# Performance work log

Measured on AMD Instinct MI355X. Metric: run time of the kernel, lower is better.

## Reference

```python
import jax, jax.numpy as jnp
import numpy as np

N, E, IN, OUT = 50000, 800000, 256, 256
EPS = 1e-5


def setup_inputs() -> dict:
    key = jax.random.key(0)
    k1, k2, k3 = jax.random.split(key, 3)
    x = jax.random.normal(k1, (N, IN), dtype=jnp.float32)
    edge_index = jax.random.randint(k2, (2, E), 0, N, dtype=jnp.int64)
    batch = jnp.zeros((N,), dtype=jnp.int64)
    # glorot-style init for GCN weight
    scale = jnp.sqrt(2.0 / (IN + OUT)).astype(jnp.float32)
    W = jax.random.normal(k3, (IN, OUT), dtype=jnp.float32) * scale
    conv_bias = jnp.zeros((OUT,), dtype=jnp.float32)
    ln_weight = jnp.ones((OUT,), dtype=jnp.float32)
    ln_bias = jnp.zeros((OUT,), dtype=jnp.float32)
    prelu_a = jnp.full((1,), 0.25, dtype=jnp.float32)  # nn.PReLU default
    return {"x": x, "edge_index": edge_index, "batch": batch, "W": W,
            "conv_bias": conv_bias, "ln_weight": ln_weight,
            "ln_bias": ln_bias, "prelu_a": prelu_a}


def reference(x, edge_index, batch, W, conv_bias, ln_weight, ln_bias, prelu_a):
    n = x.shape[0]
    src, dst = edge_index[0], edge_index[1]
    # GCNConv: add self-loops, symmetric deg^{-1/2} normalization
    loop = jnp.arange(n, dtype=src.dtype)
    src_f = jnp.concatenate([src, loop])  # [E+N]
    dst_f = jnp.concatenate([dst, loop])
    h = x @ W  # [N, OUT] -- transform before propagate (PyG order)
    deg = jax.ops.segment_sum(jnp.ones_like(dst_f, dtype=h.dtype), dst_f,
                              num_segments=n)  # >=1 due to self loops
    dinv = jax.lax.rsqrt(deg)
    norm = dinv[src_f] * dinv[dst_f]  # [E+N]
    out = jax.ops.segment_sum(h[src_f] * norm[:, None], dst_f,
                              num_segments=n) + conv_bias  # [N, OUT]
    # PyG LayerNorm, mode='graph', batch=None: normalize over ALL nodes+feats
    mu = out.mean()
    xc = out - mu
    std = jnp.sqrt((xc * xc).mean())
    y = xc / (std + EPS) * ln_weight + ln_bias
    # PReLU (single shared slope)
    return jnp.where(y >= 0, y, prelu_a * y)
```

## Files before the change

### kernel.cpp

```cpp
#include <hip/hip_runtime.h>
#include <hip/hip_bf16.h>


#define F 256
#define EPSV 1e-5f

typedef __attribute__((ext_vector_type(8))) short short8;
typedef __attribute__((ext_vector_type(8))) unsigned short ushort8v;
typedef __attribute__((ext_vector_type(4))) float f32x4;

__device__ __forceinline__ unsigned short f2bf(float f) {
  union { float f; unsigned u; } v; v.f = f;
  unsigned r = v.u + 0x7fffu + ((v.u >> 16) & 1u);
  return (unsigned short)(r >> 16);
}

__device__ __forceinline__ float bf2f(unsigned short u) {
  union { unsigned u; float f; } v; v.u = ((unsigned)u) << 16; return v.f;
}


__global__ void init_prep(int* __restrict__ deg_cnt, int N, int NB,
                          const float* __restrict__ W, unsigned short* __restrict__ Wb) {
  if ((int)blockIdx.x < NB) {
    int i = blockIdx.x * 256 + threadIdx.x;
    if (i < N) deg_cnt[i] = 0;
    return;
  }
  int gid = (blockIdx.x - NB) * 256 + threadIdx.x;
  int j = gid & 7;
  int lane = (gid >> 3) & 63;
  int kc = (gid >> 9) & 7;
  int tt = gid >> 12;
  int k = kc * 32 + (lane >> 4) * 8 + j;
  int n = tt * 16 + (lane & 15);
  Wb[gid] = f2bf(W[k * 256 + n]);
}


__global__ void count_gemm(const int* __restrict__ dst, int* __restrict__ deg_cnt,
                           int* __restrict__ rank, int E, int eb,
                           const float* __restrict__ x, const unsigned short* __restrict__ Wb,
                           ushort4* __restrict__ hb, int N) {
  __shared__ unsigned short A[64][264];

  if ((int)blockIdx.x < eb) {
    int e = blockIdx.x * 256 + threadIdx.x;
    if (e < E) rank[e] = atomicAdd(&deg_cnt[dst[e]], 1);
    return;
  }

  int m0 = (blockIdx.x - eb) * 64;
  int t = threadIdx.x;
  int lane = t & 63;
  int wave = t >> 6;
  int q = lane >> 4;

#pragma unroll
  for (int j = 0; j < 16; ++j) {
    int idx = j * 256 + t;
    int row = idx >> 6;
    int c4 = idx & 63;
    int gr = m0 + row;
    int grc = gr < N ? gr : N - 1;
    f32x4 v = __builtin_nontemporal_load((const f32x4*)(x + (size_t)grc * F + c4 * 4));
    ushort4 u;
    u.x = f2bf(v[0]); u.y = f2bf(v[1]); u.z = f2bf(v[2]); u.w = f2bf(v[3]);
    *(ushort4*)&A[row][c4 * 4] = u;
  }
  __syncthreads();

  f32x4 acc[4][4];
#pragma unroll
  for (int m = 0; m < 4; ++m)
#pragma unroll
    for (int tt = 0; tt < 4; ++tt)
      acc[m][tt] = (f32x4){0.f, 0.f, 0.f, 0.f};

  int arow = lane & 15;
  for (int kc = 0; kc < 8; ++kc) {
    short8 a[4];
#pragma unroll
    for (int m = 0; m < 4; ++m)
      a[m] = *(const short8*)&A[m * 16 + arow][kc * 32 + q * 8];
#pragma unroll
    for (int tt = 0; tt < 4; ++tt) {
      const short8 b = *(const short8*)(Wb + (((wave * 4 + tt) * 8 + kc) * 64 + lane) * 8);
#pragma unroll
      for (int m = 0; m < 4; ++m)
        acc[m][tt] = __builtin_amdgcn_mfma_f32_16x16x32_bf16(a[m], b, acc[m][tt], 0, 0, 0);
    }
  }
  __syncthreads();

  int ccol = lane & 15;
#pragma unroll
  for (int m = 0; m < 4; ++m) {
#pragma unroll
    for (int rr = 0; rr < 4; ++rr) {
      int lrow = m * 16 + q * 4 + rr;
#pragma unroll
      for (int tt = 0; tt < 4; ++tt)
        A[lrow][(wave * 4 + tt) * 16 + ccol] = f2bf(acc[m][tt][rr]);
    }
  }
  __syncthreads();
#pragma unroll
  for (int j = 0; j < 16; ++j) {
    int idx = j * 256 + t;
    int row = idx >> 6;
    int c4 = idx & 63;
    int grow = m0 + row;
    if (grow < N) hb[(size_t)grow * 64 + c4] = *(const ushort4*)&A[row][c4 * 4];
  }
}


__global__ void block_sums(const int* __restrict__ deg_cnt, int* __restrict__ bsum,
                           float* __restrict__ dinv, int N) {
  __shared__ int s[256];
  int t = threadIdx.x;
  int i = blockIdx.x * 256 + t;
  int d = (i < N) ? deg_cnt[i] : 0;
  if (i < N) dinv[i] = rsqrtf((float)(d + 1));
  s[t] = d;
  __syncthreads();
  for (int off = 128; off > 0; off >>= 1) {
    if (t < off) s[t] += s[t + off];
    __syncthreads();
  }
  if (t == 0) bsum[blockIdx.x] = s[0];
}

__global__ void scan_bsums(const int* __restrict__ bsum, int* __restrict__ boff, int nb) {
  __shared__ int s[256];
  int t = threadIdx.x;
  int v = (t < nb) ? bsum[t] : 0;
  s[t] = v;
  __syncthreads();
  for (int off = 1; off < 256; off <<= 1) {
    int x = (t >= off) ? s[t - off] : 0;
    __syncthreads();
    s[t] += x;
    __syncthreads();
  }
  if (t < nb) boff[t] = s[t] - v;
}

__global__ void write_csr(const int* __restrict__ deg_cnt, const int* __restrict__ boff,
                          int* __restrict__ csr_ptr, int N, int E) {
  __shared__ int s[256];
  int t = threadIdx.x;
  int i = blockIdx.x * 256 + t;
  int v = (i < N) ? deg_cnt[i] : 0;
  s[t] = v;
  __syncthreads();
  for (int off = 1; off < 256; off <<= 1) {
    int x = (t >= off) ? s[t - off] : 0;
    __syncthreads();
    s[t] += x;
    __syncthreads();
  }
  if (i < N) csr_ptr[i] = boff[blockIdx.x] + s[t] - v;
  if (i == 0) csr_ptr[N] = E;
}


__global__ void fill(const int* __restrict__ src, const int* __restrict__ dst,
                     const int* __restrict__ rank, const int* __restrict__ csr_ptr,
                     int* __restrict__ csr_src, int E) {
  int e = blockIdx.x * 256 + threadIdx.x;
  if (e < E) {
    int d = dst[e];
    csr_src[csr_ptr[d] + rank[e]] = src[e];
  }
}


__global__ void aggregate(const ushort4* __restrict__ hb, const int* __restrict__ csr_ptr,
                          const int* __restrict__ csr_src, const float* __restrict__ dinv,
                          const float* __restrict__ conv_bias, float* __restrict__ out,
                          double2* __restrict__ partials, int N) {
  int wave = threadIdx.x >> 6;
  int lane = threadIdx.x & 63;
  int half = lane >> 5;
  int l = lane & 31;
  int row = blockIdx.x * 8 + wave * 2 + half;
  float s1 = 0.f, s2 = 0.f;
  const unsigned short* hbs = (const unsigned short*)hb;

  if (row < N) {
    float di = dinv[row];
    int b0 = csr_ptr[row], b1 = csr_ptr[row + 1];
    ushort8v sv = *(const ushort8v*)(hbs + (size_t)row * 256 + l * 8);
    float acc[8];
#pragma unroll
    for (int c = 0; c < 8; ++c) acc[c] = bf2f(sv[c]) * di;

    for (int e = b0; e < b1; e += 8) {
      int idx[8];
#pragma unroll
      for (int j = 0; j < 8; ++j) {
        int ee = e + j;
        idx[j] = csr_src[ee < b1 ? ee : b1 - 1];
      }
      ushort8v v[8];
#pragma unroll
      for (int j = 0; j < 8; ++j)
        v[j] = *(const ushort8v*)(hbs + (size_t)idx[j] * 256 + l * 8);
      float w[8];
#pragma unroll
      for (int j = 0; j < 8; ++j) w[j] = dinv[idx[j]];
#pragma unroll
      for (int j = 0; j < 8; ++j) {
        float m = (e + j < b1) ? w[j] : 0.f;
#pragma unroll
        for (int c = 0; c < 8; ++c)
          acc[c] = fmaf(bf2f(v[j][c]), m, acc[c]);
      }
    }

    const f32x4 ba = *(const f32x4*)(conv_bias + l * 8);
    const f32x4 bb = *(const f32x4*)(conv_bias + l * 8 + 4);
    f32x4 o0, o1;
#pragma unroll
    for (int c = 0; c < 4; ++c) {
      o0[c] = fmaf(acc[c], di, ba[c]);
      o1[c] = fmaf(acc[c + 4], di, bb[c]);
    }
    float* orow = out + (size_t)row * 256 + l * 8;
    __builtin_nontemporal_store(o0, (f32x4*)orow);
    __builtin_nontemporal_store(o1, (f32x4*)(orow + 4));
#pragma unroll
    for (int c = 0; c < 4; ++c) {
      s1 += o0[c] + o1[c];
      s2 += o0[c] * o0[c] + o1[c] * o1[c];
    }
  }

  __shared__ float r1[256];
  __shared__ float r2[256];
  int t = threadIdx.x;
  r1[t] = s1;
  r2[t] = s2;
  __syncthreads();
  for (int off = 128; off > 0; off >>= 1) {
    if (t < off) { r1[t] += r1[t + off]; r2[t] += r2[t + off]; }
    __syncthreads();
  }
  if (t == 0) {
    double2 pp;
    pp.x = (double)r1[0];
    pp.y = (double)r2[0];
    partials[blockIdx.x] = pp;
  }
}


__global__ void norm_prelu(float* __restrict__ out, const double2* __restrict__ partials,
                           int nb, const float* __restrict__ lw, const float* __restrict__ lb,
                           const float* __restrict__ pa, int n4, double cnt) {
  __shared__ double q1[1024];
  __shared__ double q2[1024];
  __shared__ float sstats[2];
  int t = threadIdx.x;
  double a1 = 0.0, a2 = 0.0;
  for (int i = t; i < nb; i += 1024) {
    double2 pp = partials[i];
    a1 += pp.x;
    a2 += pp.y;
  }
  q1[t] = a1;
  q2[t] = a2;
  __syncthreads();
  for (int off = 512; off > 0; off >>= 1) {
    if (t < off) { q1[t] += q1[t + off]; q2[t] += q2[t + off]; }
    __syncthreads();
  }
  if (t == 0) {
    double mu = q1[0] / cnt;
    double var = q2[0] / cnt - mu * mu;
    if (var < 0) var = 0;
    sstats[0] = (float)mu;
    sstats[1] = (float)(1.0 / (sqrt(var) + (double)EPSV));
  }
  __syncthreads();
  float mu = sstats[0];
  float inv = sstats[1];
  float a = pa[0];
  int stride = gridDim.x * 1024;
  for (int i = blockIdx.x * 1024 + t; i < n4; i += stride) {
    int c4 = (i & 63) * 4;
    const f32x4 w = *(const f32x4*)(lw + c4);
    const f32x4 b = *(const f32x4*)(lb + c4);
    f32x4 v = __builtin_nontemporal_load((const f32x4*)(out + (size_t)i * 4));
    f32x4 y;
#pragma unroll
    for (int j = 0; j < 4; ++j) {
      float yv = (v[j] - mu) * inv * w[j] + b[j];
      y[j] = yv >= 0.f ? yv : a * yv;
    }
    __builtin_nontemporal_store(y, (f32x4*)(out + (size_t)i * 4));
  }
}


extern "C" void kernel_launch(void* const* d_in, const int* in_sizes, int n_in,
                              void* d_out, int out_size, void* d_ws, size_t ws_size,
                              hipStream_t stream) {
  const float* x = (const float*)d_in[0];
  const int* eidx = (const int*)d_in[1];
  const float* W = (const float*)d_in[3];
  const float* conv_bias = (const float*)d_in[4];
  const float* ln_w = (const float*)d_in[5];
  const float* ln_b = (const float*)d_in[6];
  const float* prelu_a = (const float*)d_in[7];
  float* out = (float*)d_out;

  int N = in_sizes[0] / F;
  int E = in_sizes[1] / 2;
  const int* src = eidx;
  const int* dst = eidx + E;

  int nAggBlocks = (N + 7) / 8;
  int eb = (E + 255) / 256;
  int gemmb = (N + 63) / 64;
  int NB = (N + 255) / 256;

  char* p = (char*)d_ws;
  auto carve = [&](size_t bytes) { char* r = p; p += (bytes + 255) & ~(size_t)255; return r; };
  ushort4* hb    = (ushort4*)carve((size_t)N * 64 * sizeof(ushort4));
  unsigned short* Wb = (unsigned short*)carve((size_t)F * F * sizeof(short));
  int* deg_cnt   = (int*)carve((size_t)N * sizeof(int));
  int* rank      = (int*)carve((size_t)E * sizeof(int));
  float* dinv    = (float*)carve((size_t)N * sizeof(float));
  int* csr_ptr   = (int*)carve((size_t)(N + 1) * sizeof(int));
  int* csr_src   = (int*)carve((size_t)E * sizeof(int));
  int* bsum      = (int*)carve((size_t)NB * sizeof(int));
  int* boff      = (int*)carve((size_t)NB * sizeof(int));
  double2* partials = (double2*)carve((size_t)nAggBlocks * sizeof(double2));

  init_prep<<<NB + 256, 256, 0, stream>>>(deg_cnt, N, NB, W, Wb);
  count_gemm<<<eb + gemmb, 256, 0, stream>>>(dst, deg_cnt, rank, E, eb, x, Wb, hb, N);
  block_sums<<<NB, 256, 0, stream>>>(deg_cnt, bsum, dinv, N);
  scan_bsums<<<1, 256, 0, stream>>>(bsum, boff, NB);
  write_csr<<<NB, 256, 0, stream>>>(deg_cnt, boff, csr_ptr, N, E);
  fill<<<eb, 256, 0, stream>>>(src, dst, rank, csr_ptr, csr_src, E);
  aggregate<<<nAggBlocks, 256, 0, stream>>>(hb, csr_ptr, csr_src, dinv,
                                            conv_bias, out, partials, N);
  int n4 = N * (F / 4);
  norm_prelu<<<256, 1024, 0, stream>>>(out, partials, nAggBlocks, ln_w, ln_b, prelu_a,
                                       n4, (double)N * (double)F);
}
```

Baseline: 268.2 us.

## Halve GEMM LDS tile, merge scan kernels, pack dst and rank

The GEMM part of count_gemm now stages x in two 32-row halves, which halves shared memory per block (64x264 to 32x264 shorts). This should raise occupancy, at the cost of extra barriers. The block-offset scan is folded into write_csr: every block redundantly scans bsum, which removes one kernel launch. The count phase packs the destination node (17 bits) and its atomic rank into one int, so fill reads one array instead of both dst and rank. The packing assumes N fits in 17 bits and the rank in 14 bits.

```diff
diff --git a/kernel.cpp b/kernel.cpp
--- a/kernel.cpp
+++ b/kernel.cpp
@@ -39,14 +39,18 @@
 
 
 __global__ void count_gemm(const int* __restrict__ dst, int* __restrict__ deg_cnt,
-                           int* __restrict__ rank, int E, int eb,
+                           int* __restrict__ packed, int E, int eb,
                            const float* __restrict__ x, const unsigned short* __restrict__ Wb,
                            ushort4* __restrict__ hb, int N) {
-  __shared__ unsigned short A[64][264];
+  __shared__ unsigned short A[32][264];
 
   if ((int)blockIdx.x < eb) {
     int e = blockIdx.x * 256 + threadIdx.x;
-    if (e < E) rank[e] = atomicAdd(&deg_cnt[dst[e]], 1);
+    if (e < E) {
+      int d = dst[e];
+      int pos = atomicAdd(&deg_cnt[d], 1);
+      packed[e] = (pos << 17) | d;
+    }
     return;
   }
 
@@ -55,20 +59,7 @@
   int lane = t & 63;
   int wave = t >> 6;
   int q = lane >> 4;
-
-#pragma unroll
-  for (int j = 0; j < 16; ++j) {
-    int idx = j * 256 + t;
-    int row = idx >> 6;
-    int c4 = idx & 63;
-    int gr = m0 + row;
-    int grc = gr < N ? gr : N - 1;
-    f32x4 v = __builtin_nontemporal_load((const f32x4*)(x + (size_t)grc * F + c4 * 4));
-    ushort4 u;
-    u.x = f2bf(v[0]); u.y = f2bf(v[1]); u.z = f2bf(v[2]); u.w = f2bf(v[3]);
-    *(ushort4*)&A[row][c4 * 4] = u;
-  }
-  __syncthreads();
+  int arow = lane & 15;
 
   f32x4 acc[4][4];
 #pragma unroll
@@ -77,41 +68,61 @@
     for (int tt = 0; tt < 4; ++tt)
       acc[m][tt] = (f32x4){0.f, 0.f, 0.f, 0.f};
 
-  int arow = lane & 15;
-  for (int kc = 0; kc < 8; ++kc) {
-    short8 a[4];
-#pragma unroll
-    for (int m = 0; m < 4; ++m)
-      a[m] = *(const short8*)&A[m * 16 + arow][kc * 32 + q * 8];
-#pragma unroll
-    for (int tt = 0; tt < 4; ++tt) {
-      const short8 b = *(const short8*)(Wb + (((wave * 4 + tt) * 8 + kc) * 64 + lane) * 8);
-#pragma unroll
-      for (int m = 0; m < 4; ++m)
-        acc[m][tt] = __builtin_amdgcn_mfma_f32_16x16x32_bf16(a[m], b, acc[m][tt], 0, 0, 0);
-    }
-  }
-  __syncthreads();
+#pragma unroll
+  for (int half = 0; half < 2; ++half) {
+#pragma unroll
+    for (int j = 0; j < 8; ++j) {
+      int idx = j * 256 + t;
+      int row = idx >> 6;
+      int c4 = idx & 63;
+      int gr = m0 + half * 32 + row;
+      int grc = gr < N ? gr : N - 1;
+      f32x4 v = __builtin_nontemporal_load((const f32x4*)(x + (size_t)grc * F + c4 * 4));
+      ushort4 u;
+      u.x = f2bf(v[0]); u.y = f2bf(v[1]); u.z = f2bf(v[2]); u.w = f2bf(v[3]);
+      *(ushort4*)&A[row][c4 * 4] = u;
+    }
+    __syncthreads();
+
+    for (int kc = 0; kc < 8; ++kc) {
+      short8 a[2];
+#pragma unroll
+      for (int m = 0; m < 2; ++m)
+        a[m] = *(const short8*)&A[m * 16 + arow][kc * 32 + q * 8];
+#pragma unroll
+      for (int tt = 0; tt < 4; ++tt) {
+        const short8 b = *(const short8*)(Wb + (((wave * 4 + tt) * 8 + kc) * 64 + lane) * 8);
+#pragma unroll
+        for (int m = 0; m < 2; ++m)
+          acc[half * 2 + m][tt] = __builtin_amdgcn_mfma_f32_16x16x32_bf16(a[m], b, acc[half * 2 + m][tt], 0, 0, 0);
+      }
+    }
+    __syncthreads();
+  }
 
   int ccol = lane & 15;
 #pragma unroll
-  for (int m = 0; m < 4; ++m) {
-#pragma unroll
-    for (int rr = 0; rr < 4; ++rr) {
-      int lrow = m * 16 + q * 4 + rr;
-#pragma unroll
-      for (int tt = 0; tt < 4; ++tt)
-        A[lrow][(wave * 4 + tt) * 16 + ccol] = f2bf(acc[m][tt][rr]);
-    }
-  }
-  __syncthreads();
-#pragma unroll
-  for (int j = 0; j < 16; ++j) {
-    int idx = j * 256 + t;
-    int row = idx >> 6;
-    int c4 = idx & 63;
-    int grow = m0 + row;
-    if (grow < N) hb[(size_t)grow * 64 + c4] = *(const ushort4*)&A[row][c4 * 4];
+  for (int half = 0; half < 2; ++half) {
+#pragma unroll
+    for (int mm = 0; mm < 2; ++mm) {
+#pragma unroll
+      for (int rr = 0; rr < 4; ++rr) {
+        int lrow = mm * 16 + q * 4 + rr;
+#pragma unroll
+        for (int tt = 0; tt < 4; ++tt)
+          A[lrow][(wave * 4 + tt) * 16 + ccol] = f2bf(acc[half * 2 + mm][tt][rr]);
+      }
+    }
+    __syncthreads();
+#pragma unroll
+    for (int j = 0; j < 8; ++j) {
+      int idx = j * 256 + t;
+      int row = idx >> 6;
+      int c4 = idx & 63;
+      int grow = m0 + half * 32 + row;
+      if (grow < N) hb[(size_t)grow * 64 + c4] = *(const ushort4*)&A[row][c4 * 4];
+    }
+    __syncthreads();
   }
 }
 
@@ -132,47 +143,45 @@
   if (t == 0) bsum[blockIdx.x] = s[0];
 }
 
-__global__ void scan_bsums(const int* __restrict__ bsum, int* __restrict__ boff, int nb) {
+
+__global__ void write_csr(const int* __restrict__ deg_cnt, const int* __restrict__ bsum,
+                          int* __restrict__ csr_ptr, int N, int E, int NB) {
+  __shared__ int sb[256];
   __shared__ int s[256];
   int t = threadIdx.x;
-  int v = (t < nb) ? bsum[t] : 0;
-  s[t] = v;
+  int bv = (t < NB) ? bsum[t] : 0;
+  sb[t] = bv;
   __syncthreads();
   for (int off = 1; off < 256; off <<= 1) {
-    int x = (t >= off) ? s[t - off] : 0;
-    __syncthreads();
-    s[t] += x;
-    __syncthreads();
-  }
-  if (t < nb) boff[t] = s[t] - v;
-}
-
-__global__ void write_csr(const int* __restrict__ deg_cnt, const int* __restrict__ boff,
-                          int* __restrict__ csr_ptr, int N, int E) {
-  __shared__ int s[256];
-  int t = threadIdx.x;
+    int xx = (t >= off) ? sb[t - off] : 0;
+    __syncthreads();
+    sb[t] += xx;
+    __syncthreads();
+  }
+  int boff = (blockIdx.x > 0) ? sb[blockIdx.x - 1] : 0;
   int i = blockIdx.x * 256 + t;
   int v = (i < N) ? deg_cnt[i] : 0;
   s[t] = v;
   __syncthreads();
   for (int off = 1; off < 256; off <<= 1) {
-    int x = (t >= off) ? s[t - off] : 0;
-    __syncthreads();
-    s[t] += x;
-    __syncthreads();
-  }
-  if (i < N) csr_ptr[i] = boff[blockIdx.x] + s[t] - v;
+    int xx = (t >= off) ? s[t - off] : 0;
+    __syncthreads();
+    s[t] += xx;
+    __syncthreads();
+  }
+  if (i < N) csr_ptr[i] = boff + s[t] - v;
   if (i == 0) csr_ptr[N] = E;
 }
 
 
-__global__ void fill(const int* __restrict__ src, const int* __restrict__ dst,
-                     const int* __restrict__ rank, const int* __restrict__ csr_ptr,
-                     int* __restrict__ csr_src, int E) {
+__global__ void fill(const int* __restrict__ src, const int* __restrict__ packed,
+                     const int* __restrict__ csr_ptr, int* __restrict__ csr_src, int E) {
   int e = blockIdx.x * 256 + threadIdx.x;
   if (e < E) {
-    int d = dst[e];
-    csr_src[csr_ptr[d] + rank[e]] = src[e];
+    int pk = packed[e];
+    int d = pk & 0x1FFFF;
+    int r = pk >> 17;
+    csr_src[csr_ptr[d] + r] = src[e];
   }
 }
 
@@ -332,20 +341,18 @@
   ushort4* hb    = (ushort4*)carve((size_t)N * 64 * sizeof(ushort4));
   unsigned short* Wb = (unsigned short*)carve((size_t)F * F * sizeof(short));
   int* deg_cnt   = (int*)carve((size_t)N * sizeof(int));
-  int* rank      = (int*)carve((size_t)E * sizeof(int));
+  int* packed    = (int*)carve((size_t)E * sizeof(int));
   float* dinv    = (float*)carve((size_t)N * sizeof(float));
   int* csr_ptr   = (int*)carve((size_t)(N + 1) * sizeof(int));
   int* csr_src   = (int*)carve((size_t)E * sizeof(int));
   int* bsum      = (int*)carve((size_t)NB * sizeof(int));
-  int* boff      = (int*)carve((size_t)NB * sizeof(int));
   double2* partials = (double2*)carve((size_t)nAggBlocks * sizeof(double2));
 
   init_prep<<<NB + 256, 256, 0, stream>>>(deg_cnt, N, NB, W, Wb);
-  count_gemm<<<eb + gemmb, 256, 0, stream>>>(dst, deg_cnt, rank, E, eb, x, Wb, hb, N);
+  count_gemm<<<eb + gemmb, 256, 0, stream>>>(dst, deg_cnt, packed, E, eb, x, Wb, hb, N);
   block_sums<<<NB, 256, 0, stream>>>(deg_cnt, bsum, dinv, N);
-  scan_bsums<<<1, 256, 0, stream>>>(bsum, boff, NB);
-  write_csr<<<NB, 256, 0, stream>>>(deg_cnt, boff, csr_ptr, N, E);
-  fill<<<eb, 256, 0, stream>>>(src, dst, rank, csr_ptr, csr_src, E);
+  write_csr<<<NB, 256, 0, stream>>>(deg_cnt, bsum, csr_ptr, N, E, NB);
+  fill<<<eb, 256, 0, stream>>>(src, packed, csr_ptr, csr_src, E);
   aggregate<<<nAggBlocks, 256, 0, stream>>>(hb, csr_ptr, csr_src, dinv,
                                             conv_bias, out, partials, N);
   int n4 = N * (F / 4);
```

Measured after the change: 271.1 us. No clear change (+1.0%).
